# Kernel optimization log

Measured on AMD Instinct MI355X. Metric: run time of the kernel, lower is better.

Reference implementation:

```python
import jax, jax.numpy as jnp
import numpy as np

WIDTH = 64
HEIGHT = 64
FEAT = 128
LAT = 64
NUM_SLOTS = 7


def pixel_coords(img_size):
    g = jnp.linspace(-1.0, 1.0, img_size)
    g1, g2 = jnp.meshgrid(g, g, indexing='ij')  # matches torch.meshgrid default
    return jnp.stack([g1, g2], axis=0)[None]  # (1, 2, S, S)


def clamp_pg(x, lo, hi):
    # clamp that preserves gradients (straight-through)
    return x + jax.lax.stop_gradient(jnp.clip(x, lo, hi) - x)


def setup_inputs() -> dict:
    key = jax.random.key(0)
    k0, k1, k2, k3 = jax.random.split(key, 4)
    bs = 64
    x = jax.random.normal(k0, (bs, FEAT, WIDTH, HEIGHT), jnp.float32)
    rand_pixel = jax.random.uniform(k1, (bs, 1, WIDTH, HEIGHT), jnp.float32)
    conv_w = jax.random.normal(k2, (LAT, FEAT), jnp.float32) / np.sqrt(FEAT)
    conv_b = jax.random.normal(k3, (LAT,), jnp.float32) * 0.01
    gate = jnp.asarray(0.5, jnp.float32)  # ScalarGate parameter (nonzero so c_f is non-degenerate)
    # laplacian kernel: sigma_init = 1 / (sqrt(num_slots) * log 2)
    log_sigma = jnp.asarray(np.log(1.0 / (np.sqrt(NUM_SLOTS) * np.log(2.0))), jnp.float32)
    return {'x': x, 'rand_pixel': rand_pixel, 'conv_w': conv_w, 'conv_b': conv_b,
            'gate': gate, 'log_sigma': log_sigma, 'num_cl_steps': 6}


def _forward(x, rand_pixel, conv_w, conv_b, gate, log_sigma, num_cl_steps):
    bs = x.shape[0]
    # SemiConv: gated 1x1 conv + fixed uv coordinate channels
    out = gate * (jnp.einsum('of,bfhw->bohw', conv_w, x) + conv_b[None, :, None, None])
    uv = jnp.concatenate([jnp.zeros((1, LAT - 2, WIDTH, HEIGHT), out.dtype),
                          pixel_coords(WIDTH).astype(out.dtype)], axis=1)
    c_f = out + uv                      # (bs, LAT, W, H)
    delta = out[:, -2:]                 # (bs, 2, W, H)
    sigma = jnp.exp(log_sigma)
    c_flat = c_f.reshape(bs, LAT, -1)   # (bs, LAT, W*H)
    b_idx = jnp.arange(bs)
    log_s0 = jnp.zeros((bs, 1, WIDTH, HEIGHT), c_f.dtype)

    def step(log_s, _):
        # interpolate-to-same-size is identity -> scope = exp(log_s)
        probs = (rand_pixel * jnp.exp(log_s)).reshape(bs, -1)
        idx = jnp.argmax(probs, axis=1)                 # (bs,)
        seed = c_flat[b_idx, :, idx]                    # (bs, LAT)
        diff = c_f - seed[:, :, None, None]
        dist = jnp.sqrt(clamp_pg((diff ** 2).sum(1), 1e-10, 1e10))  # euclidian (laplacian kernel)
        alpha = jnp.exp(-dist / sigma)[:, None]         # (bs, 1, W, H)
        alpha = clamp_pg(alpha, 0.01, 0.99)
        log_m = log_s + jnp.log(alpha)
        new_log_s = log_s + jnp.log1p(-alpha)
        return new_log_s, (log_m, new_log_s, seed)

    log_s_final, (log_m_steps, log_s_steps, seeds) = jax.lax.scan(
        step, log_s0, None, length=num_cl_steps)
    # log_m_k has num_cl_steps masks plus the final scope appended
    log_m_k = jnp.concatenate([log_m_steps, log_s_final[None]], axis=0)
    log_s_k = jnp.concatenate([log_s0[None], log_s_steps], axis=0)
    return log_m_k, log_s_k, c_f, delta, seeds


def reference(x, rand_pixel, conv_w, conv_b, gate, log_sigma, num_cl_steps):
    return _forward(x, rand_pixel, conv_w, conv_b, gate, log_sigma, num_cl_steps)
```

## Files before the change

### kernel.cpp

```cpp
#include <hip/hip_runtime.h>
#include <hip/hip_bf16.h>

#define NPIX 4096
#define FEAT 128
#define LAT 64
#define BS 64
#define NSTEPS 6

#define OFF_LOGM  0u
#define OFF_LOGS  1835008u
#define OFF_CF    3670016u
#define OFF_DELTA 20447232u
#define OFF_SEEDS 20971520u

typedef float f32x4 __attribute__((ext_vector_type(4)));
typedef short s16x8 __attribute__((ext_vector_type(8)));

__device__ __forceinline__ void amax_comb(float& bv, int& bi, float v, int i) {
    if (v > bv || (v == bv && i < bi)) { bv = v; bi = i; }
}

__device__ __forceinline__ short f2bf_rne(float r) {
    __hip_bfloat16 h = __float2bfloat16(r);
    return __builtin_bit_cast(short, h);
}

__device__ __forceinline__ void split2(float v, short& hi, short& lo) {
    unsigned u = __builtin_bit_cast(unsigned, v);
    hi = (short)(u >> 16);
    float hf = __builtin_bit_cast(float, u & 0xFFFF0000u);
    lo = f2bf_rne(v - hf);
}

__device__ __forceinline__ void transpose4(float4& v, int b) {
    float4 w;
    w.x = __shfl_xor(v.x, 1, 64); w.y = __shfl_xor(v.y, 1, 64);
    w.z = __shfl_xor(v.z, 1, 64); w.w = __shfl_xor(v.w, 1, 64);
    float4 u;
    if ((b & 1) == 0) u = make_float4(v.x, w.x, v.z, w.z);
    else              u = make_float4(w.y, v.y, w.w, v.w);
    float4 w2;
    w2.x = __shfl_xor(u.x, 2, 64); w2.y = __shfl_xor(u.y, 2, 64);
    w2.z = __shfl_xor(u.z, 2, 64); w2.w = __shfl_xor(u.w, 2, 64);
    if ((b & 2) == 0) v = make_float4(u.x, u.y, w2.x, w2.y);
    else              v = make_float4(w2.z, w2.w, u.z, u.w);
}

__global__ void prep_w(const float* __restrict__ w, const float* __restrict__ gate_p,
                       short* __restrict__ gwh, short* __restrict__ gwl)
{
    int i = blockIdx.x * 256 + threadIdx.x;
    float v = gate_p[0] * w[i];
    short h, l; split2(v, h, l);
    gwh[i] = h; gwl[i] = l;
}

__global__ __launch_bounds__(256, 2) void conv_mfma(
    const float* __restrict__ x, const float* __restrict__ rand_pixel,
    const float* __restrict__ bias, const float* __restrict__ gate_p,
    float* __restrict__ out,
    float* __restrict__ pval, int* __restrict__ pidx, int* __restrict__ cnt,
    const short* __restrict__ gwh, const short* __restrict__ gwl)
{
    __shared__ float sbias[64];

    const int tid  = threadIdx.x;
    const int b    = blockIdx.x >> 4;
    const int tile = blockIdx.x & 15;
    const int p0   = tile * 256;
    const int lane = tid & 63;
    const int wv   = tid >> 6;
    const int l15  = lane & 15;
    const int lg   = lane >> 4;
    const int j    = l15 & 3;

    if (tile == 0 && wv == 0 && lane < 8) cnt[b * 8 + lane] = 0;
    if (tid < 64) sbias[tid] = gate_p[0] * bias[tid];

    f32x4 acc[4][4];
    #pragma unroll
    for (int og = 0; og < 4; ++og)
        #pragma unroll
        for (int pg = 0; pg < 4; ++pg)
            acc[og][pg] = (f32x4){0.f, 0.f, 0.f, 0.f};

    const float* xq = x + (size_t)b * FEAT * NPIX
                        + (size_t)(lg * 8 + j) * NPIX
                        + p0 + wv * 64 + (l15 & ~3);

    float4 buf[2][8];

    #pragma unroll
    for (int i = 0; i < 8; ++i) {
        int pg = i >> 1, r = i & 1;
        buf[0][i] = *(const float4*)(xq + (size_t)(r * 4) * NPIX + pg * 16);
    }

    #pragma unroll
    for (int kc = 0; kc < 4; ++kc) {
        const int cur = kc & 1;
        if (kc < 3) {
            #pragma unroll
            for (int i = 0; i < 8; ++i) {
                int pg = i >> 1, r = i & 1;
                buf[cur ^ 1][i] = *(const float4*)(xq + (size_t)((kc + 1) * 32 + r * 4) * NPIX + pg * 16);
            }
        }

        s16x8 Ah[4], Al[4];
        #pragma unroll
        for (int og = 0; og < 4; ++og) {
            Ah[og] = *(const s16x8*)&gwh[(og * 16 + l15) * 128 + kc * 32 + lg * 8];
            Al[og] = *(const s16x8*)&gwl[(og * 16 + l15) * 128 + kc * 32 + lg * 8];
        }

        #pragma unroll
        for (int pg = 0; pg < 4; ++pg) {
            float4 t0 = buf[cur][pg * 2 + 0];
            float4 t1 = buf[cur][pg * 2 + 1];
            transpose4(t0, j);
            transpose4(t1, j);
            s16x8 Bh, Bl;
            short h, l;
            split2(t0.x, h, l); Bh[0] = h; Bl[0] = l;
            split2(t0.y, h, l); Bh[1] = h; Bl[1] = l;
            split2(t0.z, h, l); Bh[2] = h; Bl[2] = l;
            split2(t0.w, h, l); Bh[3] = h; Bl[3] = l;
            split2(t1.x, h, l); Bh[4] = h; Bl[4] = l;
            split2(t1.y, h, l); Bh[5] = h; Bl[5] = l;
            split2(t1.z, h, l); Bh[6] = h; Bl[6] = l;
            split2(t1.w, h, l); Bh[7] = h; Bl[7] = l;
            #pragma unroll
            for (int og = 0; og < 4; ++og) {
                acc[og][pg] = __builtin_amdgcn_mfma_f32_16x16x32_bf16(Ah[og], Bh, acc[og][pg], 0, 0, 0);
                acc[og][pg] = __builtin_amdgcn_mfma_f32_16x16x32_bf16(Ah[og], Bl, acc[og][pg], 0, 0, 0);
                acc[og][pg] = __builtin_amdgcn_mfma_f32_16x16x32_bf16(Al[og], Bh, acc[og][pg], 0, 0, 0);
            }
        }
    }

    __syncthreads();

    float* cf = out + OFF_CF + (size_t)b * LAT * NPIX;
    #pragma unroll
    for (int og = 0; og < 4; ++og) {
        #pragma unroll
        for (int pg = 0; pg < 4; ++pg) {
            #pragma unroll
            for (int r = 0; r < 4; ++r) {
                int o = og * 16 + lg * 4 + r;
                int p = p0 + wv * 64 + pg * 16 + l15;
                float v = acc[og][pg][r] + sbias[o];
                if (o == 62) {
                    out[OFF_DELTA + ((size_t)b * 2 + 0) * NPIX + p] = v;
                    v += (float)(-1.0 + 2.0 * (double)(p >> 6) / 63.0);
                } else if (o == 63) {
                    out[OFF_DELTA + ((size_t)b * 2 + 1) * NPIX + p] = v;
                    v += (float)(-1.0 + 2.0 * (double)(p & 63) / 63.0);
                }
                cf[(size_t)o * NPIX + p] = v;
            }
        }
    }

    if (wv == 0) {
        *(float4*)(out + OFF_LOGS + (size_t)b * NPIX + p0 + lane * 4) =
            make_float4(0.f, 0.f, 0.f, 0.f);
        float4 rv = *(const float4*)(rand_pixel + (size_t)b * NPIX + p0 + lane * 4);
        int pb = p0 + lane * 4;
        float bv = rv.x; int bi = pb;
        if (rv.y > bv) { bv = rv.y; bi = pb + 1; }
        if (rv.z > bv) { bv = rv.z; bi = pb + 2; }
        if (rv.w > bv) { bv = rv.w; bi = pb + 3; }
        #pragma unroll
        for (int off = 32; off > 0; off >>= 1) {
            float ov = __shfl_down(bv, off, 64);
            int   oi = __shfl_down(bi, off, 64);
            amax_comb(bv, bi, ov, oi);
        }
        if (lane == 0) { pval[blockIdx.x] = bv; pidx[blockIdx.x] = bi; }
    }
}

#define REP16(OP) OP(0) OP(1) OP(2) OP(3) OP(4) OP(5) OP(6) OP(7) \
                  OP(8) OP(9) OP(10) OP(11) OP(12) OP(13) OP(14) OP(15)

__global__ __launch_bounds__(1024) void steps_fused(
    const float* __restrict__ rand_pixel, const float* __restrict__ log_sigma_p,
    float* __restrict__ out, float* pv, int* pi, int* cnt)
{
    __shared__ float s_mv[16];
    __shared__ int   s_mi[16];
    __shared__ __align__(16) float s_seed[LAT];
    __shared__ float s_rv[16];
    __shared__ int   s_ri[16];

    const int tid  = threadIdx.x;
    const int b    = blockIdx.x >> 2;
    const int tile = blockIdx.x & 3;
    const int p    = tile * 1024 + tid;

    const float* cfb = out + OFF_CF + (size_t)b * LAT * NPIX;

#define DECLR(i) f32x4 r##i;
    REP16(DECLR)
#define LOADR(i) r##i = (f32x4){ cfb[(size_t)(4*i+0)*NPIX + p], cfb[(size_t)(4*i+1)*NPIX + p], \
                                 cfb[(size_t)(4*i+2)*NPIX + p], cfb[(size_t)(4*i+3)*NPIX + p] };
    REP16(LOADR)

    f32x4 aq = r0 * r0;
#define SQR(i) aq += r##i * r##i;
    SQR(1) SQR(2) SQR(3) SQR(4) SQR(5) SQR(6) SQR(7)
    SQR(8) SQR(9) SQR(10) SQR(11) SQR(12) SQR(13) SQR(14) SQR(15)
    const float cr2 = aq[0] + aq[1] + aq[2] + aq[3];

    const float rp    = rand_pixel[(size_t)b * NPIX + p];
    const float sigma = expf(log_sigma_p[0]);
    float ls = 0.f;

    #pragma unroll 1
    for (int s = 0; s < NSTEPS; ++s) {
        if (s > 0) {
            if (tid == 0) {
                while (__hip_atomic_load(&cnt[b * 8 + s], __ATOMIC_ACQUIRE,
                                         __HIP_MEMORY_SCOPE_AGENT) < 4)
                    __builtin_amdgcn_s_sleep(2);
            }
            __syncthreads();
        }
        const int nmerge = (s == 0) ? 16 : 4;
        if (tid < nmerge) {
            s_mv[tid] = __hip_atomic_load(&pv[(s * BS + b) * 16 + tid],
                                          __ATOMIC_RELAXED, __HIP_MEMORY_SCOPE_AGENT);
            s_mi[tid] = __hip_atomic_load(&pi[(s * BS + b) * 16 + tid],
                                          __ATOMIC_RELAXED, __HIP_MEMORY_SCOPE_AGENT);
        }
        __syncthreads();

        float bv = -1.0f; int bi = 0;
        for (int k = 0; k < nmerge; ++k) amax_comb(bv, bi, s_mv[k], s_mi[k]);

        if (tid < LAT) s_seed[tid] = cfb[(size_t)tid * NPIX + bi];
        __syncthreads();
        if (tile == 0 && tid < LAT)
            out[OFF_SEEDS + ((size_t)s * BS + b) * LAT + tid] = s_seed[tid];

        f32x4 dacc = (f32x4){0.f, 0.f, 0.f, 0.f};
        f32x4 sacc = (f32x4){0.f, 0.f, 0.f, 0.f};
#define DOT(i) { f32x4 sv = *(const f32x4*)&s_seed[4*i]; dacc += r##i * sv; sacc += sv * sv; }
        REP16(DOT)
        float dot = dacc[0] + dacc[1] + dacc[2] + dacc[3];
        float s2  = sacc[0] + sacc[1] + sacc[2] + sacc[3];
        float d2  = cr2 + s2 - 2.0f * dot;

        float dist  = sqrtf(fminf(fmaxf(d2, 1e-10f), 1e10f));
        float alpha = expf(-dist / sigma);
        alpha = fminf(fmaxf(alpha, 0.01f), 0.99f);
        float lm  = ls + logf(alpha);
        float lsn = ls + log1pf(-alpha);

        out[OFF_LOGM + ((size_t)s * BS + b) * NPIX + p]       = lm;
        out[OFF_LOGS + ((size_t)(s + 1) * BS + b) * NPIX + p] = lsn;
        ls = lsn;

        if (s == NSTEPS - 1) {
            out[OFF_LOGM + ((size_t)NSTEPS * BS + b) * NPIX + p] = lsn;
        } else {
            float prob = rp * expf(lsn);
            int   idx  = p;
            #pragma unroll
            for (int off = 32; off > 0; off >>= 1) {
                float ov = __shfl_down(prob, off, 64);
                int   oi = __shfl_down(idx, off, 64);
                amax_comb(prob, idx, ov, oi);
            }
            int lane = tid & 63, wid = tid >> 6;
            if (lane == 0) { s_rv[wid] = prob; s_ri[wid] = idx; }
            __syncthreads();
            if (tid == 0) {
                float fb = s_rv[0]; int fi = s_ri[0];
                #pragma unroll
                for (int k = 1; k < 16; ++k) amax_comb(fb, fi, s_rv[k], s_ri[k]);
                __hip_atomic_store(&pv[((s + 1) * BS + b) * 16 + tile], fb,
                                   __ATOMIC_RELAXED, __HIP_MEMORY_SCOPE_AGENT);
                __hip_atomic_store(&pi[((s + 1) * BS + b) * 16 + tile], fi,
                                   __ATOMIC_RELAXED, __HIP_MEMORY_SCOPE_AGENT);
                __hip_atomic_fetch_add(&cnt[b * 8 + s + 1], 1,
                                       __ATOMIC_RELEASE, __HIP_MEMORY_SCOPE_AGENT);
            }
        }
    }
}

__global__ __launch_bounds__(1024) void step_kernel(
    const float* __restrict__ rand_pixel, const float* __restrict__ log_sigma_p,
    float* __restrict__ out, float* pv, int* pi, int step)
{
    __shared__ float s_mv[16];
    __shared__ int   s_mi[16];
    __shared__ __align__(16) float s_seed[LAT];
    __shared__ float s_rv[16];
    __shared__ int   s_ri[16];

    const int tid  = threadIdx.x;
    const int b    = blockIdx.x >> 2;
    const int tile = blockIdx.x & 3;
    const int p    = tile * 1024 + tid;

    const float* cfb = out + OFF_CF + (size_t)b * LAT * NPIX;

    const int nmerge = (step == 0) ? 16 : 4;
    if (tid < nmerge) { s_mv[tid] = pv[(step * BS + b) * 16 + tid];
                        s_mi[tid] = pi[(step * BS + b) * 16 + tid]; }
    __syncthreads();
    float bv = -1.0f; int bi = 0;
    for (int k = 0; k < nmerge; ++k) amax_comb(bv, bi, s_mv[k], s_mi[k]);

    if (tid < LAT) s_seed[tid] = cfb[(size_t)tid * NPIX + bi];
    __syncthreads();
    if (tile == 0 && tid < LAT)
        out[OFF_SEEDS + ((size_t)step * BS + b) * LAT + tid] = s_seed[tid];

    float d2 = 0.f;
    #pragma unroll
    for (int c = 0; c < LAT; ++c) {
        float d = cfb[(size_t)c * NPIX + p] - s_seed[c];
        d2 = fmaf(d, d, d2);
    }
    float dist  = sqrtf(fminf(fmaxf(d2, 1e-10f), 1e10f));
    float sigma = expf(log_sigma_p[0]);
    float alpha = expf(-dist / sigma);
    alpha = fminf(fmaxf(alpha, 0.01f), 0.99f);

    float ls  = out[OFF_LOGS + ((size_t)step * BS + b) * NPIX + p];
    float lm  = ls + logf(alpha);
    float lsn = ls + log1pf(-alpha);

    out[OFF_LOGM + ((size_t)step * BS + b) * NPIX + p]       = lm;
    out[OFF_LOGS + ((size_t)(step + 1) * BS + b) * NPIX + p] = lsn;
    if (step == NSTEPS - 1)
        out[OFF_LOGM + ((size_t)NSTEPS * BS + b) * NPIX + p] = lsn;

    if (step < NSTEPS - 1) {
        float prob = rand_pixel[(size_t)b * NPIX + p] * expf(lsn);
        int   idx  = p;
        #pragma unroll
        for (int off = 32; off > 0; off >>= 1) {
            float ov = __shfl_down(prob, off, 64);
            int   oi = __shfl_down(idx, off, 64);
            amax_comb(prob, idx, ov, oi);
        }
        int lane = tid & 63, wid = tid >> 6;
        if (lane == 0) { s_rv[wid] = prob; s_ri[wid] = idx; }
        __syncthreads();
        if (tid == 0) {
            float fb = s_rv[0]; int fi = s_ri[0];
            #pragma unroll
            for (int k = 1; k < 16; ++k) amax_comb(fb, fi, s_rv[k], s_ri[k]);
            pv[((step + 1) * BS + b) * 16 + tile] = fb;
            pi[((step + 1) * BS + b) * 16 + tile] = fi;
        }
    }
}

extern "C" void kernel_launch(void* const* d_in, const int* in_sizes, int n_in,
                              void* d_out, int out_size, void* d_ws, size_t ws_size,
                              hipStream_t stream) {
    const float* x          = (const float*)d_in[0];
    const float* rand_pixel = (const float*)d_in[1];
    const float* w          = (const float*)d_in[2];
    const float* bias       = (const float*)d_in[3];
    const float* gate       = (const float*)d_in[4];
    const float* log_sigma  = (const float*)d_in[5];

    float* out = (float*)d_out;
    float* pv  = (float*)d_ws;
    int*   pi  = (int*)((char*)d_ws + 24576);
    int*   cnt = (int*)((char*)d_ws + 49152);
    short* gwh = (short*)((char*)d_ws + 51200);
    short* gwl = (short*)((char*)d_ws + 67584);

    prep_w<<<32, 256, 0, stream>>>(w, gate, gwh, gwl);
    conv_mfma<<<1024, 256, 0, stream>>>(x, rand_pixel, bias, gate, out,
                                        pv, pi, cnt, gwh, gwl);

    const float* a0 = rand_pixel; const float* a1 = log_sigma; float* a2 = out;
    float* a3 = pv; int* a4 = pi; int* a5 = cnt;
    void* kp[6] = {(void*)&a0, (void*)&a1, (void*)&a2, (void*)&a3, (void*)&a4, (void*)&a5};
    hipError_t e = hipLaunchCooperativeKernel((const void*)steps_fused,
                                              dim3(256), dim3(1024), kp, 0, stream);
    if (e != hipSuccess) {
        for (int s = 0; s < NSTEPS; ++s)
            step_kernel<<<256, 1024, 0, stream>>>(rand_pixel, log_sigma, out, pv, pi, s);
    }
}
```

Before: 138.5 us.

## Replace per-tile argmax partials with packed 64-bit atomicMax and shrink conv tiles

Per-tile argmax partials are now packed as (value bits, ~index) into a 64-bit word and combined with atomicMax, so consumers read one word instead of merging 16 or 4 partials. The conv kernel moves from 256 pixels per block to 64 (4096 blocks), with smaller accumulators and launch bounds raised to 4 blocks per SM for higher occupancy. Counter and atomic resets move into prep_w. The trade-offs are atomic contention and less reuse of the weight fragments per block.

Result: slower. 172.9 us (+24.8%).

```diff
diff --git a/kernel.cpp b/kernel.cpp
--- a/kernel.cpp
+++ b/kernel.cpp
@@ -15,9 +15,14 @@
 
 typedef float f32x4 __attribute__((ext_vector_type(4)));
 typedef short s16x8 __attribute__((ext_vector_type(8)));
+typedef unsigned long long u64;
 
 __device__ __forceinline__ void amax_comb(float& bv, int& bi, float v, int i) {
     if (v > bv || (v == bv && i < bi)) { bv = v; bi = i; }
+}
+
+__device__ __forceinline__ u64 pack_pi(float v, int idx) {
+    return ((u64)__builtin_bit_cast(unsigned, v) << 32) | (unsigned)(~idx);
 }
 
 __device__ __forceinline__ short f2bf_rne(float r) {
@@ -47,64 +52,56 @@
 }
 
 __global__ void prep_w(const float* __restrict__ w, const float* __restrict__ gate_p,
-                       short* __restrict__ gwh, short* __restrict__ gwl)
+                       short* __restrict__ gwh, short* __restrict__ gwl,
+                       u64* __restrict__ amax, int* __restrict__ cnt)
 {
     int i = blockIdx.x * 256 + threadIdx.x;
     float v = gate_p[0] * w[i];
     short h, l; split2(v, h, l);
     gwh[i] = h; gwl[i] = l;
-}
-
-__global__ __launch_bounds__(256, 2) void conv_mfma(
+    if (i < NSTEPS * BS) amax[i] = 0ull;
+    if (i < BS * 8)      cnt[i]  = 0;
+}
+
+__global__ __launch_bounds__(256, 4) void conv_mfma(
     const float* __restrict__ x, const float* __restrict__ rand_pixel,
     const float* __restrict__ bias, const float* __restrict__ gate_p,
-    float* __restrict__ out,
-    float* __restrict__ pval, int* __restrict__ pidx, int* __restrict__ cnt,
+    float* __restrict__ out, u64* __restrict__ amax,
     const short* __restrict__ gwh, const short* __restrict__ gwl)
 {
     __shared__ float sbias[64];
 
     const int tid  = threadIdx.x;
-    const int b    = blockIdx.x >> 4;
-    const int tile = blockIdx.x & 15;
-    const int p0   = tile * 256;
+    const int b    = blockIdx.x >> 6;
+    const int t    = blockIdx.x & 63;
+    const int p0   = t * 64;
     const int lane = tid & 63;
     const int wv   = tid >> 6;
     const int l15  = lane & 15;
     const int lg   = lane >> 4;
     const int j    = l15 & 3;
 
-    if (tile == 0 && wv == 0 && lane < 8) cnt[b * 8 + lane] = 0;
     if (tid < 64) sbias[tid] = gate_p[0] * bias[tid];
-
-    f32x4 acc[4][4];
+    __syncthreads();
+
+    f32x4 acc[4];
     #pragma unroll
-    for (int og = 0; og < 4; ++og)
-        #pragma unroll
-        for (int pg = 0; pg < 4; ++pg)
-            acc[og][pg] = (f32x4){0.f, 0.f, 0.f, 0.f};
+    for (int og = 0; og < 4; ++og) acc[og] = (f32x4){0.f, 0.f, 0.f, 0.f};
 
     const float* xq = x + (size_t)b * FEAT * NPIX
                         + (size_t)(lg * 8 + j) * NPIX
-                        + p0 + wv * 64 + (l15 & ~3);
-
-    float4 buf[2][8];
-
-    #pragma unroll
-    for (int i = 0; i < 8; ++i) {
-        int pg = i >> 1, r = i & 1;
-        buf[0][i] = *(const float4*)(xq + (size_t)(r * 4) * NPIX + pg * 16);
-    }
+                        + p0 + wv * 16 + (l15 & ~3);
+
+    float4 buf[2][2];
+    buf[0][0] = *(const float4*)(xq);
+    buf[0][1] = *(const float4*)(xq + (size_t)4 * NPIX);
 
     #pragma unroll
     for (int kc = 0; kc < 4; ++kc) {
         const int cur = kc & 1;
         if (kc < 3) {
-            #pragma unroll
-            for (int i = 0; i < 8; ++i) {
-                int pg = i >> 1, r = i & 1;
-                buf[cur ^ 1][i] = *(const float4*)(xq + (size_t)((kc + 1) * 32 + r * 4) * NPIX + pg * 16);
-            }
+            buf[cur ^ 1][0] = *(const float4*)(xq + (size_t)((kc + 1) * 32) * NPIX);
+            buf[cur ^ 1][1] = *(const float4*)(xq + (size_t)((kc + 1) * 32 + 4) * NPIX);
         }
 
         s16x8 Ah[4], Al[4];
@@ -114,86 +111,75 @@
             Al[og] = *(const s16x8*)&gwl[(og * 16 + l15) * 128 + kc * 32 + lg * 8];
         }
 
-        #pragma unroll
-        for (int pg = 0; pg < 4; ++pg) {
-            float4 t0 = buf[cur][pg * 2 + 0];
-            float4 t1 = buf[cur][pg * 2 + 1];
-            transpose4(t0, j);
-            transpose4(t1, j);
-            s16x8 Bh, Bl;
-            short h, l;
-            split2(t0.x, h, l); Bh[0] = h; Bl[0] = l;
-            split2(t0.y, h, l); Bh[1] = h; Bl[1] = l;
-            split2(t0.z, h, l); Bh[2] = h; Bl[2] = l;
-            split2(t0.w, h, l); Bh[3] = h; Bl[3] = l;
-            split2(t1.x, h, l); Bh[4] = h; Bl[4] = l;
-            split2(t1.y, h, l); Bh[5] = h; Bl[5] = l;
-            split2(t1.z, h, l); Bh[6] = h; Bl[6] = l;
-            split2(t1.w, h, l); Bh[7] = h; Bl[7] = l;
-            #pragma unroll
-            for (int og = 0; og < 4; ++og) {
-                acc[og][pg] = __builtin_amdgcn_mfma_f32_16x16x32_bf16(Ah[og], Bh, acc[og][pg], 0, 0, 0);
-                acc[og][pg] = __builtin_amdgcn_mfma_f32_16x16x32_bf16(Ah[og], Bl, acc[og][pg], 0, 0, 0);
-                acc[og][pg] = __builtin_amdgcn_mfma_f32_16x16x32_bf16(Al[og], Bh, acc[og][pg], 0, 0, 0);
-            }
-        }
-    }
-
-    __syncthreads();
+        float4 t0 = buf[cur][0];
+        float4 t1 = buf[cur][1];
+        transpose4(t0, j);
+        transpose4(t1, j);
+        s16x8 Bh, Bl;
+        short h, l;
+        split2(t0.x, h, l); Bh[0] = h; Bl[0] = l;
+        split2(t0.y, h, l); Bh[1] = h; Bl[1] = l;
+        split2(t0.z, h, l); Bh[2] = h; Bl[2] = l;
+        split2(t0.w, h, l); Bh[3] = h; Bl[3] = l;
+        split2(t1.x, h, l); Bh[4] = h; Bl[4] = l;
+        split2(t1.y, h, l); Bh[5] = h; Bl[5] = l;
+        split2(t1.z, h, l); Bh[6] = h; Bl[6] = l;
+        split2(t1.w, h, l); Bh[7] = h; Bl[7] = l;
+
+        #pragma unroll
+        for (int og = 0; og < 4; ++og) {
+            acc[og] = __builtin_amdgcn_mfma_f32_16x16x32_bf16(Ah[og], Bh, acc[og], 0, 0, 0);
+            acc[og] = __builtin_amdgcn_mfma_f32_16x16x32_bf16(Ah[og], Bl, acc[og], 0, 0, 0);
+            acc[og] = __builtin_amdgcn_mfma_f32_16x16x32_bf16(Al[og], Bh, acc[og], 0, 0, 0);
+        }
+    }
 
     float* cf = out + OFF_CF + (size_t)b * LAT * NPIX;
+    const int p = p0 + wv * 16 + l15;
     #pragma unroll
     for (int og = 0; og < 4; ++og) {
         #pragma unroll
-        for (int pg = 0; pg < 4; ++pg) {
-            #pragma unroll
-            for (int r = 0; r < 4; ++r) {
-                int o = og * 16 + lg * 4 + r;
-                int p = p0 + wv * 64 + pg * 16 + l15;
-                float v = acc[og][pg][r] + sbias[o];
-                if (o == 62) {
-                    out[OFF_DELTA + ((size_t)b * 2 + 0) * NPIX + p] = v;
-                    v += (float)(-1.0 + 2.0 * (double)(p >> 6) / 63.0);
-                } else if (o == 63) {
-                    out[OFF_DELTA + ((size_t)b * 2 + 1) * NPIX + p] = v;
-                    v += (float)(-1.0 + 2.0 * (double)(p & 63) / 63.0);
-                }
-                cf[(size_t)o * NPIX + p] = v;
+        for (int r = 0; r < 4; ++r) {
+            int o = og * 16 + lg * 4 + r;
+            float v = acc[og][r] + sbias[o];
+            if (o == 62) {
+                out[OFF_DELTA + ((size_t)b * 2 + 0) * NPIX + p] = v;
+                v += (float)(-1.0 + 2.0 * (double)(p >> 6) / 63.0);
+            } else if (o == 63) {
+                out[OFF_DELTA + ((size_t)b * 2 + 1) * NPIX + p] = v;
+                v += (float)(-1.0 + 2.0 * (double)(p & 63) / 63.0);
             }
+            cf[(size_t)o * NPIX + p] = v;
         }
     }
 
     if (wv == 0) {
-        *(float4*)(out + OFF_LOGS + (size_t)b * NPIX + p0 + lane * 4) =
-            make_float4(0.f, 0.f, 0.f, 0.f);
-        float4 rv = *(const float4*)(rand_pixel + (size_t)b * NPIX + p0 + lane * 4);
-        int pb = p0 + lane * 4;
-        float bv = rv.x; int bi = pb;
-        if (rv.y > bv) { bv = rv.y; bi = pb + 1; }
-        if (rv.z > bv) { bv = rv.z; bi = pb + 2; }
-        if (rv.w > bv) { bv = rv.w; bi = pb + 3; }
+        if (lane < 16)
+            *(float4*)(out + OFF_LOGS + (size_t)b * NPIX + p0 + lane * 4) =
+                make_float4(0.f, 0.f, 0.f, 0.f);
+        float bv = rand_pixel[(size_t)b * NPIX + p0 + lane];
+        int   bi = p0 + lane;
         #pragma unroll
         for (int off = 32; off > 0; off >>= 1) {
             float ov = __shfl_down(bv, off, 64);
             int   oi = __shfl_down(bi, off, 64);
             amax_comb(bv, bi, ov, oi);
         }
-        if (lane == 0) { pval[blockIdx.x] = bv; pidx[blockIdx.x] = bi; }
+        if (lane == 0) atomicMax(&amax[b], pack_pi(bv, bi));
     }
 }
 
 #define REP16(OP) OP(0) OP(1) OP(2) OP(3) OP(4) OP(5) OP(6) OP(7) \
                   OP(8) OP(9) OP(10) OP(11) OP(12) OP(13) OP(14) OP(15)
 
-__global__ __launch_bounds__(1024) void steps_fused(
+__global__ __launch_bounds__(1024, 4) void steps_fused(
     const float* __restrict__ rand_pixel, const float* __restrict__ log_sigma_p,
-    float* __restrict__ out, float* pv, int* pi, int* cnt)
+    float* __restrict__ out, u64* amax, int* cnt)
 {
-    __shared__ float s_mv[16];
-    __shared__ int   s_mi[16];
     __shared__ __align__(16) float s_seed[LAT];
     __shared__ float s_rv[16];
     __shared__ int   s_ri[16];
+    __shared__ u64   s_m;
 
     const int tid  = threadIdx.x;
     const int b    = blockIdx.x >> 2;
@@ -228,17 +214,11 @@
             }
             __syncthreads();
         }
-        const int nmerge = (s == 0) ? 16 : 4;
-        if (tid < nmerge) {
-            s_mv[tid] = __hip_atomic_load(&pv[(s * BS + b) * 16 + tid],
-                                          __ATOMIC_RELAXED, __HIP_MEMORY_SCOPE_AGENT);
-            s_mi[tid] = __hip_atomic_load(&pi[(s * BS + b) * 16 + tid],
-                                          __ATOMIC_RELAXED, __HIP_MEMORY_SCOPE_AGENT);
-        }
+        if (tid == 0)
+            s_m = __hip_atomic_load(&amax[s * BS + b], __ATOMIC_RELAXED,
+                                    __HIP_MEMORY_SCOPE_AGENT);
         __syncthreads();
-
-        float bv = -1.0f; int bi = 0;
-        for (int k = 0; k < nmerge; ++k) amax_comb(bv, bi, s_mv[k], s_mi[k]);
+        const int bi = ~(unsigned)(s_m & 0xFFFFFFFFu);
 
         if (tid < LAT) s_seed[tid] = cfb[(size_t)tid * NPIX + bi];
         __syncthreads();
@@ -281,10 +261,7 @@
                 float fb = s_rv[0]; int fi = s_ri[0];
                 #pragma unroll
                 for (int k = 1; k < 16; ++k) amax_comb(fb, fi, s_rv[k], s_ri[k]);
-                __hip_atomic_store(&pv[((s + 1) * BS + b) * 16 + tile], fb,
-                                   __ATOMIC_RELAXED, __HIP_MEMORY_SCOPE_AGENT);
-                __hip_atomic_store(&pi[((s + 1) * BS + b) * 16 + tile], fi,
-                                   __ATOMIC_RELAXED, __HIP_MEMORY_SCOPE_AGENT);
+                atomicMax(&amax[(s + 1) * BS + b], pack_pi(fb, fi));
                 __hip_atomic_fetch_add(&cnt[b * 8 + s + 1], 1,
                                        __ATOMIC_RELEASE, __HIP_MEMORY_SCOPE_AGENT);
             }
@@ -292,12 +269,10 @@
     }
 }
 
-__global__ __launch_bounds__(1024) void step_kernel(
+__global__ __launch_bounds__(1024, 4) void step_kernel(
     const float* __restrict__ rand_pixel, const float* __restrict__ log_sigma_p,
-    float* __restrict__ out, float* pv, int* pi, int step)
+    float* __restrict__ out, u64* amax, int step)
 {
-    __shared__ float s_mv[16];
-    __shared__ int   s_mi[16];
     __shared__ __align__(16) float s_seed[LAT];
     __shared__ float s_rv[16];
     __shared__ int   s_ri[16];
@@ -309,12 +284,8 @@
 
     const float* cfb = out + OFF_CF + (size_t)b * LAT * NPIX;
 
-    const int nmerge = (step == 0) ? 16 : 4;
-    if (tid < nmerge) { s_mv[tid] = pv[(step * BS + b) * 16 + tid];
-                        s_mi[tid] = pi[(step * BS + b) * 16 + tid]; }
-    __syncthreads();
-    float bv = -1.0f; int bi = 0;
-    for (int k = 0; k < nmerge; ++k) amax_comb(bv, bi, s_mv[k], s_mi[k]);
+    u64 m = amax[step * BS + b];
+    const int bi = ~(unsigned)(m & 0xFFFFFFFFu);
 
     if (tid < LAT) s_seed[tid] = cfb[(size_t)tid * NPIX + bi];
     __syncthreads();
@@ -357,8 +328,7 @@
             float fb = s_rv[0]; int fi = s_ri[0];
             #pragma unroll
             for (int k = 1; k < 16; ++k) amax_comb(fb, fi, s_rv[k], s_ri[k]);
-            pv[((step + 1) * BS + b) * 16 + tile] = fb;
-            pi[((step + 1) * BS + b) * 16 + tile] = fi;
+            atomicMax(&amax[(step + 1) * BS + b], pack_pi(fb, fi));
         }
     }
 }
@@ -374,23 +344,21 @@
     const float* log_sigma  = (const float*)d_in[5];
 
     float* out = (float*)d_out;
-    float* pv  = (float*)d_ws;
-    int*   pi  = (int*)((char*)d_ws + 24576);
-    int*   cnt = (int*)((char*)d_ws + 49152);
-    short* gwh = (short*)((char*)d_ws + 51200);
-    short* gwl = (short*)((char*)d_ws + 67584);
-
-    prep_w<<<32, 256, 0, stream>>>(w, gate, gwh, gwl);
-    conv_mfma<<<1024, 256, 0, stream>>>(x, rand_pixel, bias, gate, out,
-                                        pv, pi, cnt, gwh, gwl);
+    short* gwh  = (short*)d_ws;
+    short* gwl  = (short*)((char*)d_ws + 16384);
+    u64*   amax = (u64*)((char*)d_ws + 32768);
+    int*   cnt  = (int*)((char*)d_ws + 35840);
+
+    prep_w<<<32, 256, 0, stream>>>(w, gate, gwh, gwl, amax, cnt);
+    conv_mfma<<<4096, 256, 0, stream>>>(x, rand_pixel, bias, gate, out, amax, gwh, gwl);
 
     const float* a0 = rand_pixel; const float* a1 = log_sigma; float* a2 = out;
-    float* a3 = pv; int* a4 = pi; int* a5 = cnt;
-    void* kp[6] = {(void*)&a0, (void*)&a1, (void*)&a2, (void*)&a3, (void*)&a4, (void*)&a5};
+    u64* a3 = amax; int* a4 = cnt;
+    void* kp[5] = {(void*)&a0, (void*)&a1, (void*)&a2, (void*)&a3, (void*)&a4};
     hipError_t e = hipLaunchCooperativeKernel((const void*)steps_fused,
                                               dim3(256), dim3(1024), kp, 0, stream);
     if (e != hipSuccess) {
         for (int s = 0; s < NSTEPS; ++s)
-            step_kernel<<<256, 1024, 0, stream>>>(rand_pixel, log_sigma, out, pv, pi, s);
-    }
-}
+            step_kernel<<<256, 1024, 0, stream>>>(rand_pixel, log_sigma, out, amax, s);
+    }
+}
```

## Stage split bf16 inputs and weights in LDS, use 512-thread conv blocks

Applied to the files above, without the earlier changes.

The conv kernel now converts each x chunk to hi/lo bf16 once and writes it to LDS transposed, and it stages the split weights in LDS as well. Doubling the block to 512 threads splits output channels across two wave halves, so each wave holds half the accumulators. Before this, every wave did its own transpose and split, and read weights straight from global memory. In exchange the kernel uses about 70KB of LDS per block and adds barriers inside the K loop, which may limit occupancy and serialize load against compute.

After: 131.7 us. -4.9%, faster.

```diff
diff --git a/kernel.cpp b/kernel.cpp
--- a/kernel.cpp
+++ b/kernel.cpp
@@ -55,13 +55,17 @@
     gwh[i] = h; gwl[i] = l;
 }
 
-__global__ __launch_bounds__(256, 2) void conv_mfma(
+__global__ __launch_bounds__(512, 4) void conv_mfma(
     const float* __restrict__ x, const float* __restrict__ rand_pixel,
     const float* __restrict__ bias, const float* __restrict__ gate_p,
     float* __restrict__ out,
     float* __restrict__ pval, int* __restrict__ pidx, int* __restrict__ cnt,
     const short* __restrict__ gwh, const short* __restrict__ gwl)
 {
+    __shared__ __align__(16) short Xhi[256][40];
+    __shared__ __align__(16) short Xlo[256][40];
+    __shared__ __align__(16) short Whi[64][132];
+    __shared__ __align__(16) short Wlo[64][132];
     __shared__ float sbias[64];
 
     const int tid  = threadIdx.x;
@@ -72,93 +76,116 @@
     const int wv   = tid >> 6;
     const int l15  = lane & 15;
     const int lg   = lane >> 4;
-    const int j    = l15 & 3;
-
-    if (tile == 0 && wv == 0 && lane < 8) cnt[b * 8 + lane] = 0;
+    const int oh   = wv >> 2;
+    const int pxq  = wv & 3;
+
+    const int q  = tid >> 2;
+    const int j  = tid & 3;
+    const int P  = (q & 63) * 4;
+    const int g0 = q >> 6;
+
+    if (tile == 0 && tid < 8) cnt[b * 8 + tid] = 0;
     if (tid < 64) sbias[tid] = gate_p[0] * bias[tid];
 
-    f32x4 acc[4][4];
-    #pragma unroll
-    for (int og = 0; og < 4; ++og)
+    {
+        const int o = tid >> 3, c = (tid & 7) * 16;
+        *(s16x8*)&Whi[o][c]     = *(const s16x8*)&gwh[o * 128 + c];
+        *(s16x8*)&Whi[o][c + 8] = *(const s16x8*)&gwh[o * 128 + c + 8];
+        *(s16x8*)&Wlo[o][c]     = *(const s16x8*)&gwl[o * 128 + c];
+        *(s16x8*)&Wlo[o][c + 8] = *(const s16x8*)&gwl[o * 128 + c + 8];
+    }
+
+    const float* xb = x + (size_t)b * FEAT * NPIX + p0;
+    float4 v[4];
+    #pragma unroll
+    for (int i = 0; i < 4; ++i) {
+        int g = g0 + 2 * i;
+        v[i] = *(const float4*)(xb + (size_t)(g * 4 + j) * NPIX + P);
+    }
+    #pragma unroll
+    for (int i = 0; i < 4; ++i) {
+        int g = g0 + 2 * i;
+        float4 t = v[i]; transpose4(t, j);
+        short h0, l0, h1, l1, h2, l2, h3, l3;
+        split2(t.x, h0, l0); split2(t.y, h1, l1);
+        split2(t.z, h2, l2); split2(t.w, h3, l3);
+        *(short4*)&Xhi[P + j][g * 4] = make_short4(h0, h1, h2, h3);
+        *(short4*)&Xlo[P + j][g * 4] = make_short4(l0, l1, l2, l3);
+    }
+    __syncthreads();
+
+    f32x4 acc[2][4];
+    #pragma unroll
+    for (int og2 = 0; og2 < 2; ++og2)
         #pragma unroll
         for (int pg = 0; pg < 4; ++pg)
-            acc[og][pg] = (f32x4){0.f, 0.f, 0.f, 0.f};
-
-    const float* xq = x + (size_t)b * FEAT * NPIX
-                        + (size_t)(lg * 8 + j) * NPIX
-                        + p0 + wv * 64 + (l15 & ~3);
-
-    float4 buf[2][8];
-
-    #pragma unroll
-    for (int i = 0; i < 8; ++i) {
-        int pg = i >> 1, r = i & 1;
-        buf[0][i] = *(const float4*)(xq + (size_t)(r * 4) * NPIX + pg * 16);
-    }
+            acc[og2][pg] = (f32x4){0.f, 0.f, 0.f, 0.f};
 
     #pragma unroll
     for (int kc = 0; kc < 4; ++kc) {
-        const int cur = kc & 1;
         if (kc < 3) {
             #pragma unroll
-            for (int i = 0; i < 8; ++i) {
-                int pg = i >> 1, r = i & 1;
-                buf[cur ^ 1][i] = *(const float4*)(xq + (size_t)((kc + 1) * 32 + r * 4) * NPIX + pg * 16);
-            }
-        }
-
-        s16x8 Ah[4], Al[4];
-        #pragma unroll
-        for (int og = 0; og < 4; ++og) {
-            Ah[og] = *(const s16x8*)&gwh[(og * 16 + l15) * 128 + kc * 32 + lg * 8];
-            Al[og] = *(const s16x8*)&gwl[(og * 16 + l15) * 128 + kc * 32 + lg * 8];
+            for (int i = 0; i < 4; ++i) {
+                int g = g0 + 2 * i;
+                v[i] = *(const float4*)(xb + (size_t)((kc + 1) * 32 + g * 4 + j) * NPIX + P);
+            }
+        }
+
+        s16x8 Ah[2], Al[2];
+        #pragma unroll
+        for (int og2 = 0; og2 < 2; ++og2) {
+            int o = oh * 32 + og2 * 16 + l15;
+            Ah[og2] = *(const s16x8*)&Whi[o][kc * 32 + lg * 8];
+            Al[og2] = *(const s16x8*)&Wlo[o][kc * 32 + lg * 8];
         }
 
         #pragma unroll
         for (int pg = 0; pg < 4; ++pg) {
-            float4 t0 = buf[cur][pg * 2 + 0];
-            float4 t1 = buf[cur][pg * 2 + 1];
-            transpose4(t0, j);
-            transpose4(t1, j);
-            s16x8 Bh, Bl;
-            short h, l;
-            split2(t0.x, h, l); Bh[0] = h; Bl[0] = l;
-            split2(t0.y, h, l); Bh[1] = h; Bl[1] = l;
-            split2(t0.z, h, l); Bh[2] = h; Bl[2] = l;
-            split2(t0.w, h, l); Bh[3] = h; Bl[3] = l;
-            split2(t1.x, h, l); Bh[4] = h; Bl[4] = l;
-            split2(t1.y, h, l); Bh[5] = h; Bl[5] = l;
-            split2(t1.z, h, l); Bh[6] = h; Bl[6] = l;
-            split2(t1.w, h, l); Bh[7] = h; Bl[7] = l;
-            #pragma unroll
-            for (int og = 0; og < 4; ++og) {
-                acc[og][pg] = __builtin_amdgcn_mfma_f32_16x16x32_bf16(Ah[og], Bh, acc[og][pg], 0, 0, 0);
-                acc[og][pg] = __builtin_amdgcn_mfma_f32_16x16x32_bf16(Ah[og], Bl, acc[og][pg], 0, 0, 0);
-                acc[og][pg] = __builtin_amdgcn_mfma_f32_16x16x32_bf16(Al[og], Bh, acc[og][pg], 0, 0, 0);
-            }
-        }
-    }
-
-    __syncthreads();
+            int pxl = pxq * 64 + pg * 16 + l15;
+            s16x8 Bh = *(const s16x8*)&Xhi[pxl][lg * 8];
+            s16x8 Bl = *(const s16x8*)&Xlo[pxl][lg * 8];
+            #pragma unroll
+            for (int og2 = 0; og2 < 2; ++og2) {
+                acc[og2][pg] = __builtin_amdgcn_mfma_f32_16x16x32_bf16(Ah[og2], Bh, acc[og2][pg], 0, 0, 0);
+                acc[og2][pg] = __builtin_amdgcn_mfma_f32_16x16x32_bf16(Ah[og2], Bl, acc[og2][pg], 0, 0, 0);
+                acc[og2][pg] = __builtin_amdgcn_mfma_f32_16x16x32_bf16(Al[og2], Bh, acc[og2][pg], 0, 0, 0);
+            }
+        }
+
+        if (kc < 3) {
+            __syncthreads();
+            #pragma unroll
+            for (int i = 0; i < 4; ++i) {
+                int g = g0 + 2 * i;
+                float4 t = v[i]; transpose4(t, j);
+                short h0, l0, h1, l1, h2, l2, h3, l3;
+                split2(t.x, h0, l0); split2(t.y, h1, l1);
+                split2(t.z, h2, l2); split2(t.w, h3, l3);
+                *(short4*)&Xhi[P + j][g * 4] = make_short4(h0, h1, h2, h3);
+                *(short4*)&Xlo[P + j][g * 4] = make_short4(l0, l1, l2, l3);
+            }
+            __syncthreads();
+        }
+    }
 
     float* cf = out + OFF_CF + (size_t)b * LAT * NPIX;
     #pragma unroll
-    for (int og = 0; og < 4; ++og) {
+    for (int og2 = 0; og2 < 2; ++og2) {
         #pragma unroll
         for (int pg = 0; pg < 4; ++pg) {
             #pragma unroll
             for (int r = 0; r < 4; ++r) {
-                int o = og * 16 + lg * 4 + r;
-                int p = p0 + wv * 64 + pg * 16 + l15;
-                float v = acc[og][pg][r] + sbias[o];
+                int o = oh * 32 + og2 * 16 + lg * 4 + r;
+                int p = p0 + pxq * 64 + pg * 16 + l15;
+                float vv = acc[og2][pg][r] + sbias[o];
                 if (o == 62) {
-                    out[OFF_DELTA + ((size_t)b * 2 + 0) * NPIX + p] = v;
-                    v += (float)(-1.0 + 2.0 * (double)(p >> 6) / 63.0);
+                    out[OFF_DELTA + ((size_t)b * 2 + 0) * NPIX + p] = vv;
+                    vv += (float)(-1.0 + 2.0 * (double)(p >> 6) / 63.0);
                 } else if (o == 63) {
-                    out[OFF_DELTA + ((size_t)b * 2 + 1) * NPIX + p] = v;
-                    v += (float)(-1.0 + 2.0 * (double)(p & 63) / 63.0);
+                    out[OFF_DELTA + ((size_t)b * 2 + 1) * NPIX + p] = vv;
+                    vv += (float)(-1.0 + 2.0 * (double)(p & 63) / 63.0);
                 }
-                cf[(size_t)o * NPIX + p] = v;
+                cf[(size_t)o * NPIX + p] = vv;
             }
         }
     }
@@ -381,7 +408,7 @@
     short* gwl = (short*)((char*)d_ws + 67584);
 
     prep_w<<<32, 256, 0, stream>>>(w, gate, gwh, gwl);
-    conv_mfma<<<1024, 256, 0, stream>>>(x, rand_pixel, bias, gate, out,
+    conv_mfma<<<1024, 512, 0, stream>>>(x, rand_pixel, bias, gate, out,
                                         pv, pi, cnt, gwh, gwl);
 
     const float* a0 = rand_pixel; const float* a1 = log_sigma; float* a2 = out;
```
